# Kernel optimization log

Measured on AMD Instinct MI355X. Metric: run time of the kernel, lower is better.

Reference implementation:

```python
import jax, jax.numpy as jnp
import numpy as np

NUM_HEADS = 16
D_MODEL = 1024


def setup_inputs() -> dict:
    key = jax.random.key(0)
    ks = jax.random.split(key, 12)
    B, S, D = 2, 2048, D_MODEL
    inp = {
        "query": jax.random.normal(ks[0], (B, S, D), dtype=jnp.float32),
        "key": jax.random.normal(ks[1], (B, S, D), dtype=jnp.float32),
        "value": jax.random.normal(ks[2], (B, S, D), dtype=jnp.float32),
        "mask": jax.random.randint(ks[3], (B, 1, S), 0, 2).astype(jnp.bool_),
    }
    # Linear layer params, stored as (in, out) so y = x @ W + b
    sd = 1.0 / np.sqrt(D)
    for i, nm in enumerate(["q", "k", "v", "o"]):
        inp[f"W{nm}"] = jax.random.uniform(ks[4 + 2 * i], (D, D), jnp.float32, -sd, sd)
        inp[f"b{nm}"] = jax.random.uniform(ks[5 + 2 * i], (D,), jnp.float32, -sd, sd)
    return inp


def _split_heads(x):
    # [B, S, D] -> [B, H, S, d_k]
    B, S, D = x.shape
    return x.reshape(B, S, NUM_HEADS, D // NUM_HEADS).transpose(0, 2, 1, 3)


def reference(query, key, value, mask, Wq, bq, Wk, bk, Wv, bv, Wo, bo):
    B, Sq, D = query.shape
    d_k = D // NUM_HEADS
    scale = 1.0 / np.sqrt(d_k)

    q = _split_heads(query @ Wq + bq)   # [B,H,Sq,dk]
    k = _split_heads(key @ Wk + bk)     # [B,H,Sk,dk]
    v = _split_heads(value @ Wv + bv)   # [B,H,Sk,dk]

    scores = jnp.einsum("bhqd,bhkd->bhqk", q, k) * scale  # [B,H,Sq,Sk]
    # mask: [B,1,Sk] bool, True = masked; broadcast over heads and queries
    scores = jnp.where(mask[:, None, :, :], -jnp.inf, scores)
    attn = jax.nn.softmax(scores, axis=-1)
    attn = jnp.nan_to_num(attn, nan=0.0)  # fully-masked rows -> 0 (matches torch)

    ctx = jnp.einsum("bhqk,bhkd->bhqd", attn, v)  # [B,H,Sq,dk]
    ctx = ctx.transpose(0, 2, 1, 3).reshape(B, Sq, D)  # combine heads
    out = ctx @ Wo + bo
    return out
```

## Files before the change

kernel.cpp:

```cpp
#include <hip/hip_runtime.h>


typedef unsigned short u16;
typedef __attribute__((ext_vector_type(8))) short bf16x8;
typedef __attribute__((ext_vector_type(4))) float f32x4;

static __device__ __forceinline__ u16 f2bf(float x) {
  union { float f; unsigned int i; } v; v.f = x;
  return (u16)((v.i + 0x8000u) >> 16);
}
static __device__ __forceinline__ float bf2f(u16 u) {
  union { unsigned int i; float f; } v; v.i = ((unsigned int)u) << 16; return v.f;
}

#define MFMA_B16(a, b, c) __builtin_amdgcn_mfma_f32_16x16x32_bf16((a), (b), (c), 0, 0, 0)

__global__ __launch_bounds__(256) void prep_w(
    const float* __restrict__ w0, const float* __restrict__ w1,
    const float* __restrict__ w2, const float* __restrict__ w3,
    u16* __restrict__ t0, u16* __restrict__ t1,
    u16* __restrict__ t2, u16* __restrict__ t3) {
  __shared__ u16 tile[64 * 68];
  const float* W; u16* T;
  switch (blockIdx.z) {
    case 0: W = w0; T = t0; break;
    case 1: W = w1; T = t1; break;
    case 2: W = w2; T = t2; break;
    default: W = w3; T = t3; break;
  }
  const int t = threadIdx.x;
  const int k0 = blockIdx.x * 64, n0 = blockIdx.y * 64;
#pragma unroll
  for (int it = 0; it < 4; ++it) {
    int idx = it * 256 + t;
    int r = idx >> 4, c4 = idx & 15;
    float4 v = *(const float4*)&W[(size_t)(k0 + r) * 1024 + n0 + c4 * 4];
    tile[r * 68 + c4 * 4 + 0] = f2bf(v.x);
    tile[r * 68 + c4 * 4 + 1] = f2bf(v.y);
    tile[r * 68 + c4 * 4 + 2] = f2bf(v.z);
    tile[r * 68 + c4 * 4 + 3] = f2bf(v.w);
  }
  __syncthreads();
#pragma unroll
  for (int it = 0; it < 2; ++it) {
    int idx = it * 256 + t;
    int n = idx >> 3, kc = idx & 7;
    bf16x8 pk;
#pragma unroll
    for (int j = 0; j < 8; ++j) pk[j] = (short)tile[(kc * 8 + j) * 68 + n];
    *(bf16x8*)&T[(size_t)(n0 + n) * 1024 + k0 + kc * 8] = pk;
  }
}

template <int MT, int AMODE, int OMODE>
__global__ __launch_bounds__(256) void gemm_bias(
    const void* a0v, const void* a1v, const void* a2v,
    const u16* __restrict__ Wt,
    const float* b0, const float* b1, const float* b2,
    void* o0, void* o1, void* o2) {
  __shared__ __align__(16) u16 As[MT * 32 * 32];
  __shared__ __align__(16) u16 Bs[128 * 32];
  const int t = threadIdx.x, wave = t >> 6, lane = t & 63;
  const int l15 = lane & 15, quad = lane >> 4;
  const int m0 = blockIdx.x * (MT * 32);
  const int n0 = blockIdx.y * 128;
  const int rg = (OMODE == 3) ? (n0 >> 10) : 0;
  const void* Av = (rg == 0) ? a0v : (rg == 1 ? a1v : a2v);
  const float* bp = (rg == 0) ? b0 : (rg == 1 ? b1 : b2);
  const int nb = (OMODE == 3) ? (n0 & 1023) : n0;
  const int wr = (wave >> 1) * (MT * 16), wc = (wave & 1) * 64;

  const f32x4 fz = {0.f, 0.f, 0.f, 0.f};
  f32x4 acc[MT][4];
#pragma unroll
  for (int mt = 0; mt < MT; ++mt)
#pragma unroll
    for (int nt = 0; nt < 4; ++nt) acc[mt][nt] = fz;

  float4 pa[MT / 2][2]; bf16x8 pab[MT / 2]; bf16x8 pb[2];
#pragma unroll
  for (int s = 0; s < MT / 2; ++s) {
    int idx = s * 256 + t, row = idx >> 2, seg = idx & 3;
    if (AMODE == 1) {
      const float* ap = (const float*)Av + (size_t)(m0 + row) * 1024 + seg * 8;
      pa[s][0] = *(const float4*)ap; pa[s][1] = *(const float4*)(ap + 4);
    } else {
      pab[s] = *(const bf16x8*)((const u16*)Av + (size_t)(m0 + row) * 1024 + seg * 8);
    }
  }
#pragma unroll
  for (int s = 0; s < 2; ++s) {
    int idx = s * 256 + t, row = idx >> 2, seg = idx & 3;
    pb[s] = *(const bf16x8*)&Wt[(size_t)(n0 + row) * 1024 + seg * 8];
  }

  for (int kb = 0; kb < 1024; kb += 32) {
    __syncthreads();
#pragma unroll
    for (int s = 0; s < MT / 2; ++s) {
      int idx = s * 256 + t, row = idx >> 2, seg = idx & 3;
      bf16x8 pk;
      if (AMODE == 1) {
        pk[0] = (short)f2bf(pa[s][0].x); pk[1] = (short)f2bf(pa[s][0].y);
        pk[2] = (short)f2bf(pa[s][0].z); pk[3] = (short)f2bf(pa[s][0].w);
        pk[4] = (short)f2bf(pa[s][1].x); pk[5] = (short)f2bf(pa[s][1].y);
        pk[6] = (short)f2bf(pa[s][1].z); pk[7] = (short)f2bf(pa[s][1].w);
      } else pk = pab[s];
      *(bf16x8*)&As[row * 32 + seg * 8] = pk;
    }
#pragma unroll
    for (int s = 0; s < 2; ++s) {
      int idx = s * 256 + t, row = idx >> 2, seg = idx & 3;
      *(bf16x8*)&Bs[row * 32 + seg * 8] = pb[s];
    }
    __syncthreads();
    const int kn = (kb + 32) & 1023;
#pragma unroll
    for (int s = 0; s < MT / 2; ++s) {
      int idx = s * 256 + t, row = idx >> 2, seg = idx & 3;
      if (AMODE == 1) {
        const float* ap = (const float*)Av + (size_t)(m0 + row) * 1024 + kn + seg * 8;
        pa[s][0] = *(const float4*)ap; pa[s][1] = *(const float4*)(ap + 4);
      } else {
        pab[s] = *(const bf16x8*)((const u16*)Av + (size_t)(m0 + row) * 1024 + kn + seg * 8);
      }
    }
#pragma unroll
    for (int s = 0; s < 2; ++s) {
      int idx = s * 256 + t, row = idx >> 2, seg = idx & 3;
      pb[s] = *(const bf16x8*)&Wt[(size_t)(n0 + row) * 1024 + kn + seg * 8];
    }
    bf16x8 a[MT], bfr[4];
#pragma unroll
    for (int mt = 0; mt < MT; ++mt)
      a[mt] = *(const bf16x8*)&As[(wr + mt * 16 + l15) * 32 + quad * 8];
#pragma unroll
    for (int nt = 0; nt < 4; ++nt)
      bfr[nt] = *(const bf16x8*)&Bs[(wc + nt * 16 + l15) * 32 + quad * 8];
#pragma unroll
    for (int mt = 0; mt < MT; ++mt)
#pragma unroll
      for (int nt = 0; nt < 4; ++nt)
        acc[mt][nt] = MFMA_B16(a[mt], bfr[nt], acc[mt][nt]);
  }

#pragma unroll
  for (int nt = 0; nt < 4; ++nt) {
    const int n = nb + wc + nt * 16 + l15;
    const float bv = bp[n];
#pragma unroll
    for (int mt = 0; mt < MT; ++mt)
#pragma unroll
      for (int r = 0; r < 4; ++r) {
        const int m = m0 + wr + mt * 16 + quad * 4 + r;
        const float val = acc[mt][nt][r] + bv;
        if (OMODE == 2) {
          ((float*)o0)[(size_t)m * 1024 + n] = val;
        } else if (OMODE == 0) {
          ((u16*)o0)[(size_t)m * 1024 + n] = f2bf(val);
        } else {
          if (rg == 0)      ((u16*)o0)[(size_t)m * 1024 + n] = f2bf(val);
          else if (rg == 1) ((u16*)o1)[(size_t)m * 1024 + n] = f2bf(val);
          else {
            const int h = n >> 6, d = n & 63, bb = m >> 11, ss = m & 2047;
            ((u16*)o2)[((size_t)(bb * 16 + h) * 64 + d) * 2048 + ss] = f2bf(val);
          }
        }
      }
  }
}

__global__ __launch_bounds__(512) void attn_fused(
    const u16* Q, const u16* __restrict__ K,
    const u16* __restrict__ Vt, const int* __restrict__ mask,
    u16* ctx) {
  __shared__ __align__(16) u16 Ks[128 * 72];
  __shared__ __align__(16) u16 Vs[64 * 136];
  __shared__ __align__(16) u16 Pl[8][16 * 136];
  __shared__ u16 Mb[2048];
  const int t = threadIdx.x, wave = t >> 6, lane = t & 63;
  const int l15 = lane & 15, quad = lane >> 4;
  const int bh = blockIdx.y, b = bh >> 4, h = bh & 15;
  const int q0 = blockIdx.x * 128 + wave * 16;
  const float cs = 0.125f * 1.44269504f;

#pragma unroll
  for (int i = 0; i < 4; ++i) {
    int idx = i * 512 + t;
    Mb[idx] = mask[b * 2048 + idx] ? 0xFF80 : 0;
  }

  const u16* Qp = Q + (size_t)(b * 2048 + q0) * 1024 + h * 64;
  const bf16x8 qf0 = *(const bf16x8*)(Qp + (size_t)l15 * 1024 + quad * 8);
  const bf16x8 qf1 = *(const bf16x8*)(Qp + (size_t)l15 * 1024 + 32 + quad * 8);

  const u16* Kbase = K + (size_t)(b * 2048) * 1024 + h * 64;
  const u16* Vbase = Vt + (size_t)bh * 64 * 2048;

  const int kr0 = t >> 3,        kc0 = (t & 7) * 8;
  const int kr1 = (512 + t) >> 3;
  const int vr0 = t >> 4,        vc0 = (t & 15) * 8;
  const int vr1 = (512 + t) >> 4;

  bf16x8 gk0 = *(const bf16x8*)&Kbase[(size_t)kr0 * 1024 + kc0];
  bf16x8 gk1 = *(const bf16x8*)&Kbase[(size_t)kr1 * 1024 + kc0];
  bf16x8 gv0 = *(const bf16x8*)&Vbase[(size_t)vr0 * 2048 + vc0];
  bf16x8 gv1 = *(const bf16x8*)&Vbase[(size_t)vr1 * 2048 + vc0];

  const f32x4 fz = {0.f, 0.f, 0.f, 0.f};
  f32x4 o[4];
  f32x4 lpart = fz;
#pragma unroll
  for (int i = 0; i < 4; ++i) o[i] = fz;

  for (int kt = 0; kt < 2048; kt += 128) {
    __syncthreads();
    *(bf16x8*)&Ks[kr0 * 72 + kc0] = gk0;
    *(bf16x8*)&Ks[kr1 * 72 + kc0] = gk1;
    *(bf16x8*)&Vs[vr0 * 136 + vc0] = gv0;
    *(bf16x8*)&Vs[vr1 * 136 + vc0] = gv1;
    __syncthreads();
    const int kn = (kt + 128) & 2047;
    gk0 = *(const bf16x8*)&Kbase[(size_t)(kn + kr0) * 1024 + kc0];
    gk1 = *(const bf16x8*)&Kbase[(size_t)(kn + kr1) * 1024 + kc0];
    gv0 = *(const bf16x8*)&Vbase[(size_t)vr0 * 2048 + kn + vc0];
    gv1 = *(const bf16x8*)&Vbase[(size_t)vr1 * 2048 + kn + vc0];

    float pv[8][4];
#pragma unroll
    for (int nt = 0; nt < 8; ++nt) {
      const int krow = nt * 16 + l15;
      bf16x8 k0 = *(const bf16x8*)&Ks[krow * 72 + quad * 8];
      bf16x8 k1 = *(const bf16x8*)&Ks[krow * 72 + 32 + quad * 8];
      f32x4 acc = MFMA_B16(qf0, k0, fz);
      acc = MFMA_B16(qf1, k1, acc);
      const float bias = bf2f(Mb[kt + krow]);
#pragma unroll
      for (int r = 0; r < 4; ++r) {
        float p = exp2f(fmaf(acc[r], cs, bias));
        pv[nt][r] = p; lpart[r] += p;
      }
    }
#pragma unroll
    for (int nt = 0; nt < 8; ++nt)
#pragma unroll
      for (int r = 0; r < 4; ++r)
        Pl[wave][(quad * 4 + r) * 136 + nt * 16 + l15] = f2bf(pv[nt][r]);
#pragma unroll
    for (int kc = 0; kc < 4; ++kc) {
      const bf16x8 pf = *(const bf16x8*)&Pl[wave][l15 * 136 + kc * 32 + quad * 8];
#pragma unroll
      for (int nt = 0; nt < 4; ++nt) {
        const bf16x8 vf = *(const bf16x8*)&Vs[(nt * 16 + l15) * 136 + kc * 32 + quad * 8];
        o[nt] = MFMA_B16(pf, vf, o[nt]);
      }
    }
  }
  float lrow[4];
#pragma unroll
  for (int r = 0; r < 4; ++r) {
    float sl = lpart[r];
    sl += __shfl_xor(sl, 1);
    sl += __shfl_xor(sl, 2);
    sl += __shfl_xor(sl, 4);
    sl += __shfl_xor(sl, 8);
    lrow[r] = sl;
  }
  u16* cp = ctx + (size_t)(b * 2048 + q0) * 1024 + h * 64;
#pragma unroll
  for (int r = 0; r < 4; ++r) {
    const bool ok = lrow[r] > 0.f;
    const float inv = ok ? 1.f / lrow[r] : 0.f;
#pragma unroll
    for (int nt = 0; nt < 4; ++nt)
      cp[(quad * 4 + r) * 1024 + nt * 16 + l15] = f2bf(ok ? o[nt][r] * inv : 0.f);
  }
}

extern "C" void kernel_launch(void* const* d_in, const int* in_sizes, int n_in,
                              void* d_out, int out_size, void* d_ws, size_t ws_size,
                              hipStream_t stream) {
  const float* q    = (const float*)d_in[0];
  const float* k    = (const float*)d_in[1];
  const float* v    = (const float*)d_in[2];
  const int*   mask = (const int*)d_in[3];
  const float* Wq = (const float*)d_in[4];  const float* bq = (const float*)d_in[5];
  const float* Wk = (const float*)d_in[6];  const float* bk = (const float*)d_in[7];
  const float* Wv = (const float*)d_in[8];  const float* bv = (const float*)d_in[9];
  const float* Wo = (const float*)d_in[10]; const float* bo = (const float*)d_in[11];

  char* ws = (char*)d_ws;
  u16*   Kp  = (u16*)(ws + ((size_t)0 << 20));
  u16*   Vt  = (u16*)(ws + ((size_t)8 << 20));
  float* O32 = (float*)ws;

  char* od = (char*)d_out;
  u16* ctx = (u16*)od;
  u16* WqT = (u16*)(od + ((size_t)8 << 20));
  u16* WkT = (u16*)(od + ((size_t)10 << 20));
  u16* WvT = (u16*)(od + ((size_t)12 << 20));
  u16* WoT = (u16*)(od + ((size_t)14 << 20));

  dim3 blk(256);
  prep_w<<<dim3(16, 16, 4), blk, 0, stream>>>(Wq, Wk, Wv, Wo, WqT, WkT, WvT, WoT);
  gemm_bias<4, 1, 3><<<dim3(32, 24), blk, 0, stream>>>(
      q, k, v, WqT, bq, bk, bv, (void*)ctx, (void*)Kp, (void*)Vt);
  attn_fused<<<dim3(16, 32), dim3(512), 0, stream>>>(ctx, Kp, Vt, mask, ctx);
  gemm_bias<2, 0, 2><<<dim3(64, 8), blk, 0, stream>>>(
      ctx, nullptr, nullptr, WoT, bo, nullptr, nullptr, (void*)O32, nullptr, nullptr);
  hipMemcpyAsync(d_out, O32, (size_t)out_size * sizeof(float),
                 hipMemcpyDeviceToDevice, stream);
}
```

Measured before the change: 263.4 us.

## Double-buffer GEMM tiles via direct global-to-LDS loads and transpose attention scores

The projection GEMM now uses two LDS buffers, filled with global_load_lds for bf16 operands and packed v_cvt_pk_bf16_f32 conversion for fp32 inputs, so each iteration needs one barrier and the next tile's fill overlaps the MFMAs. The attention kernel computes S^T (K as the A operand), so each lane holds four consecutive key columns. That lets it read the mask bias as one float4, pack P with cvt_pk, write it with 8-byte LDS stores and keep a single scalar row sum. The cost is twice the GEMM LDS footprint, plus reliance on the async-LDS load semantics and the transposed fragment layout being exactly right.

```diff
diff --git a/kernel.cpp b/kernel.cpp
--- a/kernel.cpp
+++ b/kernel.cpp
@@ -4,13 +4,24 @@
 typedef unsigned short u16;
 typedef __attribute__((ext_vector_type(8))) short bf16x8;
 typedef __attribute__((ext_vector_type(4))) float f32x4;
+typedef __attribute__((ext_vector_type(4))) unsigned int u32x4;
+typedef __attribute__((ext_vector_type(2))) unsigned int u32x2;
 
 static __device__ __forceinline__ u16 f2bf(float x) {
   union { float f; unsigned int i; } v; v.f = x;
   return (u16)((v.i + 0x8000u) >> 16);
 }
-static __device__ __forceinline__ float bf2f(u16 u) {
-  union { unsigned int i; float f; } v; v.i = ((unsigned int)u) << 16; return v.f;
+
+static __device__ __forceinline__ unsigned int cvtpk(float lo, float hi) {
+  unsigned int r;
+  asm("v_cvt_pk_bf16_f32 %0, %1, %2" : "=v"(r) : "v"(lo), "v"(hi));
+  return r;
+}
+
+static __device__ __forceinline__ void gload_lds16(const u16* g, u16* l) {
+  __builtin_amdgcn_global_load_lds(
+      (const __attribute__((address_space(1))) unsigned int*)g,
+      (__attribute__((address_space(3))) unsigned int*)l, 16, 0, 0);
 }
 
 #define MFMA_B16(a, b, c) __builtin_amdgcn_mfma_f32_16x16x32_bf16((a), (b), (c), 0, 0, 0)
@@ -58,8 +69,8 @@
     const u16* __restrict__ Wt,
     const float* b0, const float* b1, const float* b2,
     void* o0, void* o1, void* o2) {
-  __shared__ __align__(16) u16 As[MT * 32 * 32];
-  __shared__ __align__(16) u16 Bs[128 * 32];
+  __shared__ __align__(16) u16 As[2][MT * 32 * 32];
+  __shared__ __align__(16) u16 Bs[2][128 * 32];
   const int t = threadIdx.x, wave = t >> 6, lane = t & 63;
   const int l15 = lane & 15, quad = lane >> 4;
   const int m0 = blockIdx.x * (MT * 32);
@@ -77,71 +88,91 @@
 #pragma unroll
     for (int nt = 0; nt < 4; ++nt) acc[mt][nt] = fz;
 
-  float4 pa[MT / 2][2]; bf16x8 pab[MT / 2]; bf16x8 pb[2];
-#pragma unroll
-  for (int s = 0; s < MT / 2; ++s) {
-    int idx = s * 256 + t, row = idx >> 2, seg = idx & 3;
-    if (AMODE == 1) {
+  float4 pa[MT / 2][2];
+
+#pragma unroll
+  for (int s = 0; s < 2; ++s) {
+    int idx = s * 256 + t;
+    gload_lds16(&Wt[(size_t)(n0 + (idx >> 2)) * 1024 + (idx & 3) * 8], &Bs[0][idx * 8]);
+  }
+  if (AMODE == 0) {
+#pragma unroll
+    for (int s = 0; s < MT / 2; ++s) {
+      int idx = s * 256 + t;
+      gload_lds16((const u16*)Av + (size_t)(m0 + (idx >> 2)) * 1024 + (idx & 3) * 8,
+                  &As[0][idx * 8]);
+    }
+  } else {
+#pragma unroll
+    for (int s = 0; s < MT / 2; ++s) {
+      int idx = s * 256 + t, row = idx >> 2, seg = idx & 3;
       const float* ap = (const float*)Av + (size_t)(m0 + row) * 1024 + seg * 8;
       pa[s][0] = *(const float4*)ap; pa[s][1] = *(const float4*)(ap + 4);
-    } else {
-      pab[s] = *(const bf16x8*)((const u16*)Av + (size_t)(m0 + row) * 1024 + seg * 8);
-    }
-  }
-#pragma unroll
-  for (int s = 0; s < 2; ++s) {
-    int idx = s * 256 + t, row = idx >> 2, seg = idx & 3;
-    pb[s] = *(const bf16x8*)&Wt[(size_t)(n0 + row) * 1024 + seg * 8];
-  }
-
-  for (int kb = 0; kb < 1024; kb += 32) {
-    __syncthreads();
+    }
+#pragma unroll
+    for (int s = 0; s < MT / 2; ++s) {
+      int idx = s * 256 + t;
+      u32x4 w;
+      w[0] = cvtpk(pa[s][0].x, pa[s][0].y); w[1] = cvtpk(pa[s][0].z, pa[s][0].w);
+      w[2] = cvtpk(pa[s][1].x, pa[s][1].y); w[3] = cvtpk(pa[s][1].z, pa[s][1].w);
+      *(u32x4*)&As[0][idx * 8] = w;
+    }
 #pragma unroll
     for (int s = 0; s < MT / 2; ++s) {
       int idx = s * 256 + t, row = idx >> 2, seg = idx & 3;
-      bf16x8 pk;
-      if (AMODE == 1) {
-        pk[0] = (short)f2bf(pa[s][0].x); pk[1] = (short)f2bf(pa[s][0].y);
-        pk[2] = (short)f2bf(pa[s][0].z); pk[3] = (short)f2bf(pa[s][0].w);
-        pk[4] = (short)f2bf(pa[s][1].x); pk[5] = (short)f2bf(pa[s][1].y);
-        pk[6] = (short)f2bf(pa[s][1].z); pk[7] = (short)f2bf(pa[s][1].w);
-      } else pk = pab[s];
-      *(bf16x8*)&As[row * 32 + seg * 8] = pk;
-    }
+      const float* ap = (const float*)Av + (size_t)(m0 + row) * 1024 + 32 + seg * 8;
+      pa[s][0] = *(const float4*)ap; pa[s][1] = *(const float4*)(ap + 4);
+    }
+  }
+  __syncthreads();
+
+  int buf = 0;
+  for (int kb = 0; kb < 1024; kb += 32) {
+    const int kn = (kb + 32) & 1023;
 #pragma unroll
     for (int s = 0; s < 2; ++s) {
-      int idx = s * 256 + t, row = idx >> 2, seg = idx & 3;
-      *(bf16x8*)&Bs[row * 32 + seg * 8] = pb[s];
-    }
-    __syncthreads();
-    const int kn = (kb + 32) & 1023;
-#pragma unroll
-    for (int s = 0; s < MT / 2; ++s) {
-      int idx = s * 256 + t, row = idx >> 2, seg = idx & 3;
-      if (AMODE == 1) {
-        const float* ap = (const float*)Av + (size_t)(m0 + row) * 1024 + kn + seg * 8;
+      int idx = s * 256 + t;
+      gload_lds16(&Wt[(size_t)(n0 + (idx >> 2)) * 1024 + kn + (idx & 3) * 8],
+                  &Bs[buf ^ 1][idx * 8]);
+    }
+    if (AMODE == 0) {
+#pragma unroll
+      for (int s = 0; s < MT / 2; ++s) {
+        int idx = s * 256 + t;
+        gload_lds16((const u16*)Av + (size_t)(m0 + (idx >> 2)) * 1024 + kn + (idx & 3) * 8,
+                    &As[buf ^ 1][idx * 8]);
+      }
+    } else {
+#pragma unroll
+      for (int s = 0; s < MT / 2; ++s) {
+        int idx = s * 256 + t;
+        u32x4 w;
+        w[0] = cvtpk(pa[s][0].x, pa[s][0].y); w[1] = cvtpk(pa[s][0].z, pa[s][0].w);
+        w[2] = cvtpk(pa[s][1].x, pa[s][1].y); w[3] = cvtpk(pa[s][1].z, pa[s][1].w);
+        *(u32x4*)&As[buf ^ 1][idx * 8] = w;
+      }
+      const int kn2 = (kb + 64) & 1023;
+#pragma unroll
+      for (int s = 0; s < MT / 2; ++s) {
+        int idx = s * 256 + t, row = idx >> 2, seg = idx & 3;
+        const float* ap = (const float*)Av + (size_t)(m0 + row) * 1024 + kn2 + seg * 8;
         pa[s][0] = *(const float4*)ap; pa[s][1] = *(const float4*)(ap + 4);
-      } else {
-        pab[s] = *(const bf16x8*)((const u16*)Av + (size_t)(m0 + row) * 1024 + kn + seg * 8);
-      }
-    }
-#pragma unroll
-    for (int s = 0; s < 2; ++s) {
-      int idx = s * 256 + t, row = idx >> 2, seg = idx & 3;
-      pb[s] = *(const bf16x8*)&Wt[(size_t)(n0 + row) * 1024 + kn + seg * 8];
+      }
     }
     bf16x8 a[MT], bfr[4];
 #pragma unroll
     for (int mt = 0; mt < MT; ++mt)
-      a[mt] = *(const bf16x8*)&As[(wr + mt * 16 + l15) * 32 + quad * 8];
+      a[mt] = *(const bf16x8*)&As[buf][(wr + mt * 16 + l15) * 32 + quad * 8];
 #pragma unroll
     for (int nt = 0; nt < 4; ++nt)
-      bfr[nt] = *(const bf16x8*)&Bs[(wc + nt * 16 + l15) * 32 + quad * 8];
+      bfr[nt] = *(const bf16x8*)&Bs[buf][(wc + nt * 16 + l15) * 32 + quad * 8];
 #pragma unroll
     for (int mt = 0; mt < MT; ++mt)
 #pragma unroll
       for (int nt = 0; nt < 4; ++nt)
         acc[mt][nt] = MFMA_B16(a[mt], bfr[nt], acc[mt][nt]);
+    __syncthreads();
+    buf ^= 1;
   }
 
 #pragma unroll
@@ -177,7 +208,7 @@
   __shared__ __align__(16) u16 Ks[128 * 72];
   __shared__ __align__(16) u16 Vs[64 * 136];
   __shared__ __align__(16) u16 Pl[8][16 * 136];
-  __shared__ u16 Mb[2048];
+  __shared__ __align__(16) float Mf[2048];
   const int t = threadIdx.x, wave = t >> 6, lane = t & 63;
   const int l15 = lane & 15, quad = lane >> 4;
   const int bh = blockIdx.y, b = bh >> 4, h = bh & 15;
@@ -187,7 +218,7 @@
 #pragma unroll
   for (int i = 0; i < 4; ++i) {
     int idx = i * 512 + t;
-    Mb[idx] = mask[b * 2048 + idx] ? 0xFF80 : 0;
+    Mf[idx] = mask[b * 2048 + idx] ? -__builtin_inff() : 0.f;
   }
 
   const u16* Qp = Q + (size_t)(b * 2048 + q0) * 1024 + h * 64;
@@ -209,7 +240,7 @@
 
   const f32x4 fz = {0.f, 0.f, 0.f, 0.f};
   f32x4 o[4];
-  f32x4 lpart = fz;
+  float lsum = 0.f;
 #pragma unroll
   for (int i = 0; i < 4; ++i) o[i] = fz;
 
@@ -226,26 +257,24 @@
     gv0 = *(const bf16x8*)&Vbase[(size_t)vr0 * 2048 + kn + vc0];
     gv1 = *(const bf16x8*)&Vbase[(size_t)vr1 * 2048 + kn + vc0];
 
-    float pv[8][4];
 #pragma unroll
     for (int nt = 0; nt < 8; ++nt) {
       const int krow = nt * 16 + l15;
       bf16x8 k0 = *(const bf16x8*)&Ks[krow * 72 + quad * 8];
       bf16x8 k1 = *(const bf16x8*)&Ks[krow * 72 + 32 + quad * 8];
-      f32x4 acc = MFMA_B16(qf0, k0, fz);
-      acc = MFMA_B16(qf1, k1, acc);
-      const float bias = bf2f(Mb[kt + krow]);
-#pragma unroll
-      for (int r = 0; r < 4; ++r) {
-        float p = exp2f(fmaf(acc[r], cs, bias));
-        pv[nt][r] = p; lpart[r] += p;
-      }
-    }
-#pragma unroll
-    for (int nt = 0; nt < 8; ++nt)
-#pragma unroll
-      for (int r = 0; r < 4; ++r)
-        Pl[wave][(quad * 4 + r) * 136 + nt * 16 + l15] = f2bf(pv[nt][r]);
+      f32x4 acc = MFMA_B16(k0, qf0, fz);
+      acc = MFMA_B16(k1, qf1, acc);
+      const float4 bias4 = *(const float4*)&Mf[kt + nt * 16 + quad * 4];
+      float p0 = exp2f(fmaf(acc[0], cs, bias4.x));
+      float p1 = exp2f(fmaf(acc[1], cs, bias4.y));
+      float p2 = exp2f(fmaf(acc[2], cs, bias4.z));
+      float p3 = exp2f(fmaf(acc[3], cs, bias4.w));
+      lsum += (p0 + p1) + (p2 + p3);
+      u32x2 pp;
+      pp.x = cvtpk(p0, p1);
+      pp.y = cvtpk(p2, p3);
+      *(u32x2*)&Pl[wave][l15 * 136 + nt * 16 + quad * 4] = pp;
+    }
 #pragma unroll
     for (int kc = 0; kc < 4; ++kc) {
       const bf16x8 pf = *(const bf16x8*)&Pl[wave][l15 * 136 + kc * 32 + quad * 8];
@@ -256,21 +285,14 @@
       }
     }
   }
-  float lrow[4];
+  lsum += __shfl_xor(lsum, 16);
+  lsum += __shfl_xor(lsum, 32);
+  u16* cp = ctx + (size_t)(b * 2048 + q0) * 1024 + h * 64;
 #pragma unroll
   for (int r = 0; r < 4; ++r) {
-    float sl = lpart[r];
-    sl += __shfl_xor(sl, 1);
-    sl += __shfl_xor(sl, 2);
-    sl += __shfl_xor(sl, 4);
-    sl += __shfl_xor(sl, 8);
-    lrow[r] = sl;
-  }
-  u16* cp = ctx + (size_t)(b * 2048 + q0) * 1024 + h * 64;
-#pragma unroll
-  for (int r = 0; r < 4; ++r) {
-    const bool ok = lrow[r] > 0.f;
-    const float inv = ok ? 1.f / lrow[r] : 0.f;
+    const float lrow = __shfl(lsum, quad * 4 + r);
+    const bool ok = lrow > 0.f;
+    const float inv = ok ? 1.f / lrow : 0.f;
 #pragma unroll
     for (int nt = 0; nt < 4; ++nt)
       cp[(quad * 4 + r) * 1024 + nt * 16 + l15] = f2bf(ok ? o[nt][r] * inv : 0.f);
```

Measured after the change: 285.4 us. 8.4% more time.
